# Optimization experiments

Measured on AMD Instinct MI355X. Metric: run time of the kernel, lower is better.

## Reference

```python
import jax, jax.numpy as jnp
import numpy as np
import math

B, S, D_MODEL, N_HEAD, D_HEAD, D_FFN = 1, 2048, 1024, 16, 64, 4096
EPS = 1e-6


def setup_inputs() -> dict:
    key = jax.random.key(0)
    ks = jax.random.split(key, 10)
    scale = 0.02
    x = jax.random.normal(ks[0], (B, S, D_MODEL), dtype=jnp.float32)
    # RoPE frequencies: freqs_cis[s, i] = exp(1j * s * theta_i), theta_i = 10000^{-2i/d_head}
    half = D_HEAD // 2
    inv_freq = 1.0 / (10000.0 ** (jnp.arange(0, half, dtype=jnp.float32) * 2.0 / D_HEAD))
    angles = jnp.arange(S, dtype=jnp.float32)[:, None] * inv_freq[None, :]  # [S, half]
    freqs_cos = jnp.cos(angles)
    freqs_sin = jnp.sin(angles)
    wq = jax.random.normal(ks[1], (D_MODEL, N_HEAD * D_HEAD), dtype=jnp.float32) * scale
    wk = jax.random.normal(ks[2], (D_MODEL, N_HEAD * D_HEAD), dtype=jnp.float32) * scale
    wv = jax.random.normal(ks[3], (D_MODEL, N_HEAD * D_HEAD), dtype=jnp.float32) * scale
    wo = jax.random.normal(ks[4], (N_HEAD * D_HEAD, D_MODEL), dtype=jnp.float32) * scale
    w1 = jax.random.normal(ks[5], (D_MODEL, D_FFN), dtype=jnp.float32) * scale
    w2 = jax.random.normal(ks[6], (D_FFN, D_MODEL), dtype=jnp.float32) * scale
    w3 = jax.random.normal(ks[7], (D_MODEL, D_FFN), dtype=jnp.float32) * scale
    attn_norm_w = jnp.ones((D_MODEL,), dtype=jnp.float32)
    ffn_norm_w = jnp.ones((D_MODEL,), dtype=jnp.float32)
    return {"x": x, "freqs_cos": freqs_cos, "freqs_sin": freqs_sin,
            "wq": wq, "wk": wk, "wv": wv, "wo": wo,
            "w1": w1, "w2": w2, "w3": w3,
            "attn_norm_w": attn_norm_w, "ffn_norm_w": ffn_norm_w}


def _rmsnorm(x, w):
    xf = x.astype(jnp.float32)
    inv = jax.lax.rsqrt(jnp.mean(xf * xf, axis=-1, keepdims=True) + EPS)
    return (xf * inv).astype(x.dtype) * w


def _rope(t, cos, sin):
    # t: [B, S, H, D]; treat last dim as interleaved (even, odd) complex pairs
    b, s, h, d = t.shape
    tr = t.astype(jnp.float32).reshape(b, s, h, d // 2, 2)
    te, to = tr[..., 0], tr[..., 1]
    c = cos[None, :, None, :]
    sn = sin[None, :, None, :]
    out = jnp.stack([te * c - to * sn, te * sn + to * c], axis=-1)
    return out.reshape(b, s, h, d).astype(t.dtype)


def reference(x, freqs_cos, freqs_sin, wq, wk, wv, wo, w1, w2, w3, attn_norm_w, ffn_norm_w):
    bsz, seqlen, _ = x.shape
    # --- attention sub-block ---
    hin = _rmsnorm(x, attn_norm_w)
    q = (hin @ wq).reshape(bsz, seqlen, N_HEAD, D_HEAD)
    k = (hin @ wk).reshape(bsz, seqlen, N_HEAD, D_HEAD)
    v = (hin @ wv).reshape(bsz, seqlen, N_HEAD, D_HEAD)
    q = _rope(q, freqs_cos, freqs_sin)
    k = _rope(k, freqs_cos, freqs_sin)
    # [B, H, S, S] scores, softmax in fp32 (no causal mask in original)
    scores = jnp.einsum('bqhd,bkhd->bhqk', q, k) / math.sqrt(D_HEAD)
    probs = jax.nn.softmax(scores.astype(jnp.float32), axis=-1).astype(q.dtype)
    attn = jnp.einsum('bhqk,bkhd->bqhd', probs, v).reshape(bsz, seqlen, N_HEAD * D_HEAD)
    h = x + attn @ wo
    # --- SwiGLU FFN sub-block ---
    f = _rmsnorm(h, ffn_norm_w)
    ffn = (jax.nn.silu(f @ w1) * (f @ w3)) @ w2
    return h + ffn
```

## Files before the change

kernel.cpp:

```cpp
#include <hip/hip_runtime.h>
#include <stdint.h>
#include <stddef.h>

using bf16x8 = __attribute__((ext_vector_type(8))) __bf16;
using f32x4  = __attribute__((ext_vector_type(4))) float;
using f32x16 = __attribute__((ext_vector_type(16))) float;

__device__ __forceinline__ float bf2f(unsigned short u) {
  union { unsigned int i; float f; } v; v.i = ((unsigned int)u) << 16; return v.f;
}
__device__ __forceinline__ unsigned short f2bf(float f) {
  union { float f; unsigned int i; } v; v.f = f;
  unsigned int r = v.i + 0x7fffu + ((v.i >> 16) & 1u);
  return (unsigned short)(r >> 16);
}
__device__ __forceinline__ unsigned short f2bf_trunc(float f) {
  union { float f; unsigned int i; } v; v.f = f;
  return (unsigned short)(v.i >> 16);
}
__device__ __forceinline__ void async16(const void* g, void* l) {
  __builtin_amdgcn_global_load_lds(
      (const __attribute__((address_space(1))) unsigned int*)g,
      (__attribute__((address_space(3))) unsigned int*)l, 16, 0, 0);
}

#define S_LEN 2048
#define DMODEL 1024
#define NHEAD 16
#define DHEAD 64
#define DFFN 4096

struct T4 {
  const float *s0, *s1, *s2, *s3;
  unsigned short *d0, *d1, *d2, *d3;
};
__global__ __launch_bounds__(256) void transpose4_k(T4 j) {
  const float* in = blockIdx.z == 0 ? j.s0 : blockIdx.z == 1 ? j.s1 : blockIdx.z == 2 ? j.s2 : j.s3;
  unsigned short* out = blockIdx.z == 0 ? j.d0 : blockIdx.z == 1 ? j.d1 : blockIdx.z == 2 ? j.d2 : j.d3;
  __shared__ unsigned short tile[32][33];
  const int tx = threadIdx.x & 31;
  const int ty = threadIdx.x >> 5;
  const int bc = blockIdx.x * 32;
  const int br = blockIdx.y * 32;
#pragma unroll
  for (int i = 0; i < 4; ++i)
    tile[ty + i * 8][tx] = f2bf(in[(size_t)(br + ty + i * 8) * 1024 + bc + tx]);
  __syncthreads();
#pragma unroll
  for (int i = 0; i < 4; ++i)
    out[(size_t)(bc + ty + i * 8) * 1024 + br + tx] = tile[tx][ty + i * 8];
}

__global__ __launch_bounds__(256) void transpose13_k(
    const float* __restrict__ w1, const float* __restrict__ w3,
    unsigned short* __restrict__ out) {
  const float* in = blockIdx.z ? w3 : w1;
  const int rb = blockIdx.z * 32;
  __shared__ unsigned short tile[32][33];
  const int tx = threadIdx.x & 31;
  const int ty = threadIdx.x >> 5;
  const int bc = blockIdx.x * 32;
  const int br = blockIdx.y * 32;
#pragma unroll
  for (int i = 0; i < 4; ++i)
    tile[ty + i * 8][tx] = f2bf(in[(size_t)(br + ty + i * 8) * 4096 + bc + tx]);
  __syncthreads();
#pragma unroll
  for (int i = 0; i < 4; ++i) {
    int c = bc + ty + i * 8;
    int dest = (c >> 5) * 64 + rb + (c & 31);
    out[(size_t)dest * 1024 + br + tx] = tile[tx][ty + i * 8];
  }
}

__global__ __launch_bounds__(256) void transpose_w2_k(
    const float* __restrict__ in, unsigned short* __restrict__ out) {
  __shared__ unsigned short tile[32][33];
  const int tx = threadIdx.x & 31;
  const int ty = threadIdx.x >> 5;
  const int bc = blockIdx.x * 32;
  const int br = blockIdx.y * 32;
#pragma unroll
  for (int i = 0; i < 4; ++i)
    tile[ty + i * 8][tx] = f2bf(in[(size_t)(br + ty + i * 8) * 1024 + bc + tx]);
  __syncthreads();
#pragma unroll
  for (int i = 0; i < 4; ++i)
    out[(size_t)(bc + ty + i * 8) * 4096 + br + tx] = tile[tx][ty + i * 8];
}

__global__ __launch_bounds__(256) void vtrans_k(
    const unsigned short* __restrict__ QKV, unsigned short* __restrict__ VtG) {
  __shared__ unsigned short tile[32][33];
  const int tx = threadIdx.x & 31;
  const int ty = threadIdx.x >> 5;
  const int bc = blockIdx.x * 32;
  const int br = blockIdx.y * 32;
#pragma unroll
  for (int i = 0; i < 4; ++i)
    tile[ty + i * 8][tx] = QKV[(size_t)(br + ty + i * 8) * 3072 + 2048 + bc + tx];
  __syncthreads();
#pragma unroll
  for (int i = 0; i < 4; ++i)
    VtG[(size_t)(bc + ty + i * 8) * 2048 + br + tx] = tile[tx][ty + i * 8];
}

__global__ __launch_bounds__(256) void rmsnorm_k(
    const float* __restrict__ X, const float* __restrict__ W,
    unsigned short* __restrict__ Y) {
  const int row = blockIdx.x;
  const int t = threadIdx.x;
  const int lane = t & 63, w = t >> 6;
  const float* x = X + (size_t)row * DMODEL;
  float xs[4];
  float s = 0.f;
#pragma unroll
  for (int i = 0; i < 4; ++i) {
    xs[i] = x[t * 4 + i];
    s += xs[i] * xs[i];
  }
#pragma unroll
  for (int m = 1; m < 64; m <<= 1) s += __shfl_xor(s, m, 64);
  __shared__ float red[4];
  if (lane == 0) red[w] = s;
  __syncthreads();
  float tot = red[0] + red[1] + red[2] + red[3];
  float inv = rsqrtf(tot * (1.0f / DMODEL) + 1e-6f);
#pragma unroll
  for (int i = 0; i < 4; ++i)
    Y[(size_t)row * DMODEL + t * 4 + i] = f2bf(xs[i] * inv * W[t * 4 + i]);
}

template <int MODE>
__global__ __launch_bounds__(256) void gemm_bt(
    const unsigned short* __restrict__ A, int lda,
    const unsigned short* __restrict__ BT,
    void* __restrict__ Cout,
    int K, int N) {
  __shared__ unsigned short As[128 * 64];
  __shared__ unsigned short Bs[128 * 64];
  const int t = threadIdx.x;
  const int lane = t & 63;
  const int w = t >> 6;
  const int qr = (w >> 1) * 64, qc = (w & 1) * 64;
  const int l31 = lane & 31, half = lane >> 5;
  const int m0 = blockIdx.y * 128, n0 = blockIdx.x * 128;

  f32x16 acc[2][2] = {};

  int srow[4], scol[4];
#pragma unroll
  for (int p = 0; p < 4; ++p) {
    int off = p * 2048 + t * 8;
    int r = off >> 6;
    srow[p] = r;
    scol[p] = (((off >> 3) & 7) ^ (r & 7)) * 8;
  }

  for (int k0 = 0; k0 < K; k0 += 64) {
    __syncthreads();
#pragma unroll
    for (int p = 0; p < 4; ++p) {
      int off = p * 2048 + t * 8;
      async16(A + (size_t)(m0 + srow[p]) * lda + (k0 + scol[p]), &As[off]);
      async16(BT + (size_t)(n0 + srow[p]) * K + (k0 + scol[p]), &Bs[off]);
    }
    __syncthreads();
#pragma unroll
    for (int ks = 0; ks < 4; ++ks) {
      const int ch = ((ks * 2 + half) ^ (l31 & 7)) * 8;
      bf16x8 a0 = *(const bf16x8*)&As[(qr + l31) * 64 + ch];
      bf16x8 a1 = *(const bf16x8*)&As[(qr + 32 + l31) * 64 + ch];
      bf16x8 b0 = *(const bf16x8*)&Bs[(qc + l31) * 64 + ch];
      bf16x8 b1 = *(const bf16x8*)&Bs[(qc + 32 + l31) * 64 + ch];
      acc[0][0] = __builtin_amdgcn_mfma_f32_32x32x16_bf16(a0, b0, acc[0][0], 0, 0, 0);
      acc[0][1] = __builtin_amdgcn_mfma_f32_32x32x16_bf16(a0, b1, acc[0][1], 0, 0, 0);
      acc[1][0] = __builtin_amdgcn_mfma_f32_32x32x16_bf16(a1, b0, acc[1][0], 0, 0, 0);
      acc[1][1] = __builtin_amdgcn_mfma_f32_32x32x16_bf16(a1, b1, acc[1][1], 0, 0, 0);
    }
  }

  if constexpr (MODE == 2) {
    unsigned short* C = (unsigned short*)Cout;
    const int ld = N >> 1;
#pragma unroll
    for (int rt = 0; rt < 2; ++rt)
#pragma unroll
      for (int reg = 0; reg < 16; ++reg) {
        int rr = m0 + qr + rt * 32 + (reg & 3) + 8 * (reg >> 2) + 4 * half;
        int cc = ((n0 + qc) >> 1) + l31;
        float a1v = acc[rt][0][reg];
        float a3v = acc[rt][1][reg];
        float f = a1v / (1.f + __expf(-a1v)) * a3v;
        C[(size_t)rr * ld + cc] = f2bf(f);
      }
  } else {
    unsigned short* C = (unsigned short*)Cout;
#pragma unroll
    for (int rt = 0; rt < 2; ++rt)
#pragma unroll
      for (int ct = 0; ct < 2; ++ct)
#pragma unroll
        for (int reg = 0; reg < 16; ++reg) {
          int rr = m0 + qr + rt * 32 + (reg & 3) + 8 * (reg >> 2) + 4 * half;
          int cc = n0 + qc + ct * 32 + l31;
          C[(size_t)rr * N + cc] = f2bf(acc[rt][ct][reg]);
        }
  }
}

struct PtrPair { float* p0; float* p1; };

__global__ __launch_bounds__(256) void gemm_bt_sk(
    const unsigned short* __restrict__ A, int lda,
    const unsigned short* __restrict__ BT,
    PtrPair parts, int Kc, int Ktot, int N) {
  __shared__ unsigned short As[64 * 64];
  __shared__ unsigned short Bs[128 * 64];
  const int t = threadIdx.x;
  const int lane = t & 63;
  const int w = t >> 6;
  const int qr = (w >> 1) * 32, qc = (w & 1) * 64;
  const int l31 = lane & 31, half = lane >> 5;
  const int m0 = blockIdx.y * 64, n0 = blockIdx.x * 128;
  const int kb = blockIdx.z * Kc;

  f32x16 acc[2] = {};

  for (int k0 = 0; k0 < Kc; k0 += 64) {
    __syncthreads();
#pragma unroll
    for (int p = 0; p < 2; ++p) {
      int off = p * 2048 + t * 8;
      int r = off >> 6;
      int sc = (((off >> 3) & 7) ^ (r & 7)) * 8;
      async16(A + (size_t)(m0 + r) * lda + (kb + k0 + sc), &As[off]);
    }
#pragma unroll
    for (int p = 0; p < 4; ++p) {
      int off = p * 2048 + t * 8;
      int r = off >> 6;
      int sc = (((off >> 3) & 7) ^ (r & 7)) * 8;
      async16(BT + (size_t)(n0 + r) * Ktot + (kb + k0 + sc), &Bs[off]);
    }
    __syncthreads();
#pragma unroll
    for (int ks = 0; ks < 4; ++ks) {
      const int ch = ((ks * 2 + half) ^ (l31 & 7)) * 8;
      bf16x8 a0 = *(const bf16x8*)&As[(qr + l31) * 64 + ch];
      bf16x8 b0 = *(const bf16x8*)&Bs[(qc + l31) * 64 + ch];
      bf16x8 b1 = *(const bf16x8*)&Bs[(qc + 32 + l31) * 64 + ch];
      acc[0] = __builtin_amdgcn_mfma_f32_32x32x16_bf16(a0, b0, acc[0], 0, 0, 0);
      acc[1] = __builtin_amdgcn_mfma_f32_32x32x16_bf16(a0, b1, acc[1], 0, 0, 0);
    }
  }

  float* C = blockIdx.z ? parts.p1 : parts.p0;
#pragma unroll
  for (int ct = 0; ct < 2; ++ct)
#pragma unroll
    for (int reg = 0; reg < 16; ++reg) {
      int rr = m0 + qr + (reg & 3) + 8 * (reg >> 2) + 4 * half;
      int cc = n0 + qc + ct * 32 + l31;
      C[(size_t)rr * N + cc] = acc[ct][reg];
    }
}

__global__ __launch_bounds__(256) void reduce2_k(
    const float4* __restrict__ P0, const float4* __restrict__ P1,
    const float4* __restrict__ R, float4* __restrict__ Out, int nvec) {
  int i = blockIdx.x * 256 + threadIdx.x;
  if (i >= nvec) return;
  float4 a = P0[i], b = P1[i], r = R[i];
  float4 o;
  o.x = a.x + b.x + r.x;
  o.y = a.y + b.y + r.y;
  o.z = a.z + b.z + r.z;
  o.w = a.w + b.w + r.w;
  Out[i] = o;
}

__global__ __launch_bounds__(256) void rope_k(
    unsigned short* __restrict__ QKV,
    const float* __restrict__ cosp,
    const float* __restrict__ sinp) {
  int idx = blockIdx.x * 256 + threadIdx.x;
  int s = idx >> 9;
  int rem = idx & 511;
  int h = rem >> 5;
  int i = rem & 31;
  float c = cosp[s * 32 + i];
  float sn = sinp[s * 32 + i];
  size_t off = (size_t)s * 3072 + h * 64 + 2 * i;
  {
    float e = bf2f(QKV[off]), o = bf2f(QKV[off + 1]);
    QKV[off] = f2bf(e * c - o * sn);
    QKV[off + 1] = f2bf(e * sn + o * c);
  }
  {
    float e = bf2f(QKV[off + 1024]), o = bf2f(QKV[off + 1025]);
    QKV[off + 1024] = f2bf((e * c - o * sn) * 0.125f);
    QKV[off + 1025] = f2bf((e * sn + o * c) * 0.125f);
  }
}

#define VPAD 132
__device__ __forceinline__ int swz(int row, int col) { return col ^ ((row & 7) * 8); }

__global__ __launch_bounds__(256) void attn_k(
    const unsigned short* __restrict__ QKV,
    const unsigned short* __restrict__ VtG,
    float* __restrict__ O0, float* __restrict__ O1,
    float* __restrict__ L) {
  const int h = blockIdx.y;
  const int qb = blockIdx.x;
  const int z = blockIdx.z;
  const int t = threadIdx.x;
  const int lane = t & 63;
  const int w = t >> 6;
  const int row16 = lane & 15, quad = lane >> 4;
  const int q0 = qb * 64 + w * 16;
  const int kbase = z * 1024;

  __shared__ unsigned short Ks[128 * 64];
  __shared__ unsigned short Vt[64 * 128];
  __shared__ unsigned short Ps[4][16 * VPAD];

  const unsigned short* Qp = QKV;
  const unsigned short* Kp = QKV + 1024;
  const unsigned short* Vg = VtG + (size_t)h * 64 * 2048;

  bf16x8 aq[2];
#pragma unroll
  for (int kk = 0; kk < 2; ++kk)
    aq[kk] = *(const bf16x8*)(Qp + (size_t)(q0 + row16) * 3072 + h * 64 + kk * 32 + quad * 8);

  f32x4 o[4] = {};
  float l_r[4] = {0.f, 0.f, 0.f, 0.f};

  bf16x8 kreg[4], vreg[4];
#pragma unroll
  for (int p = 0; p < 4; ++p) {
    int off = p * 2048 + t * 8;
    int r = off >> 6, c = off & 63;
    kreg[p] = *(const bf16x8*)(Kp + (size_t)(kbase + r) * 3072 + h * 64 + c);
    int d = off >> 7, key = off & 127;
    vreg[p] = *(const bf16x8*)(Vg + (size_t)d * 2048 + kbase + key);
  }

  for (int kb = kbase; kb < kbase + 1024; kb += 128) {
    __syncthreads();
#pragma unroll
    for (int p = 0; p < 4; ++p) {
      int off = p * 2048 + t * 8;
      int r = off >> 6, c = off & 63;
      *(bf16x8*)&Ks[r * 64 + swz(r, c)] = kreg[p];
      int d = off >> 7, key = off & 127;
      *(bf16x8*)&Vt[d * 128 + swz(d, key)] = vreg[p];
    }
    __syncthreads();
    if (kb + 128 < kbase + 1024) {
      int kb2 = kb + 128;
#pragma unroll
      for (int p = 0; p < 4; ++p) {
        int off = p * 2048 + t * 8;
        int r = off >> 6, c = off & 63;
        kreg[p] = *(const bf16x8*)(Kp + (size_t)(kb2 + r) * 3072 + h * 64 + c);
        int d = off >> 7, key = off & 127;
        vreg[p] = *(const bf16x8*)(Vg + (size_t)d * 2048 + kb2 + key);
      }
    }

    f32x4 sc[8];
#pragma unroll
    for (int tj = 0; tj < 8; ++tj) {
      int kr = tj * 16 + row16;
      bf16x8 b0 = *(const bf16x8*)&Ks[kr * 64 + swz(kr, quad * 8)];
      bf16x8 b1 = *(const bf16x8*)&Ks[kr * 64 + swz(kr, 32 + quad * 8)];
      f32x4 z4 = {};
      z4 = __builtin_amdgcn_mfma_f32_16x16x32_bf16(aq[0], b0, z4, 0, 0, 0);
      z4 = __builtin_amdgcn_mfma_f32_16x16x32_bf16(aq[1], b1, z4, 0, 0, 0);
      sc[tj] = z4;
    }

#pragma unroll
    for (int reg = 0; reg < 4; ++reg) {
      float ssum = 0.f;
#pragma unroll
      for (int tj = 0; tj < 8; ++tj) {
        float p = __expf(sc[tj][reg]);
        sc[tj][reg] = p;
        ssum += p;
      }
#pragma unroll
      for (int m = 1; m < 16; m <<= 1) ssum += __shfl_xor(ssum, m, 16);
      l_r[reg] += ssum;
    }

#pragma unroll
    for (int tj = 0; tj < 8; ++tj)
#pragma unroll
      for (int reg = 0; reg < 4; ++reg)
        Ps[w][(quad * 4 + reg) * VPAD + tj * 16 + row16] = f2bf_trunc(sc[tj][reg]);

    bf16x8 ap[4];
#pragma unroll
    for (int kk = 0; kk < 4; ++kk)
      ap[kk] = *(const bf16x8*)&Ps[w][row16 * VPAD + kk * 32 + quad * 8];
#pragma unroll
    for (int dt = 0; dt < 4; ++dt) {
      int dr = dt * 16 + row16;
#pragma unroll
      for (int kk = 0; kk < 4; ++kk) {
        bf16x8 bv = *(const bf16x8*)&Vt[dr * 128 + swz(dr, kk * 32 + quad * 8)];
        o[dt] = __builtin_amdgcn_mfma_f32_16x16x32_bf16(ap[kk], bv, o[dt], 0, 0, 0);
      }
    }
  }

  float* Op = z ? O1 : O0;
#pragma unroll
  for (int dt = 0; dt < 4; ++dt)
#pragma unroll
    for (int reg = 0; reg < 4; ++reg)
      Op[(size_t)(q0 + quad * 4 + reg) * DMODEL + h * 64 + dt * 16 + row16] = o[dt][reg];
  if (row16 == 0)
#pragma unroll
    for (int reg = 0; reg < 4; ++reg)
      L[(size_t)(h * 2 + z) * S_LEN + q0 + quad * 4 + reg] = l_r[reg];
}

__global__ __launch_bounds__(256) void attn_combine_k(
    const float4* __restrict__ O0, const float4* __restrict__ O1,
    const float* __restrict__ L, unsigned short* __restrict__ Attn) {
  int i = blockIdx.x * 256 + threadIdx.x;
  int e0 = i * 4;
  int s = e0 >> 10;
  int c = e0 & 1023;
  int h = c >> 6;
  float la = L[(size_t)(h * 2) * S_LEN + s];
  float lb = L[(size_t)(h * 2 + 1) * S_LEN + s];
  float inv = 1.f / (la + lb);
  float4 a = O0[i], b = O1[i];
  ushort4 r;
  r.x = f2bf((a.x + b.x) * inv);
  r.y = f2bf((a.y + b.y) * inv);
  r.z = f2bf((a.z + b.z) * inv);
  r.w = f2bf((a.w + b.w) * inv);
  *(ushort4*)(Attn + e0) = r;
}

extern "C" void kernel_launch(void* const* d_in, const int* in_sizes, int n_in,
                              void* d_out, int out_size, void* d_ws, size_t ws_size,
                              hipStream_t stream) {
  (void)in_sizes; (void)n_in; (void)out_size; (void)ws_size;
  const float* x    = (const float*)d_in[0];
  const float* fcos = (const float*)d_in[1];
  const float* fsin = (const float*)d_in[2];
  const float* wq   = (const float*)d_in[3];
  const float* wk   = (const float*)d_in[4];
  const float* wv   = (const float*)d_in[5];
  const float* wo   = (const float*)d_in[6];
  const float* w1   = (const float*)d_in[7];
  const float* w2   = (const float*)d_in[8];
  const float* w3   = (const float*)d_in[9];
  const float* anw  = (const float*)d_in[10];
  const float* fnw  = (const float*)d_in[11];
  float* out = (float*)d_out;
  char* ws = (char*)d_ws;

  unsigned short* WqkvT = (unsigned short*)(ws + 0);
  unsigned short* VtG   = (unsigned short*)(ws + 0);
  float*          Lbuf  = (float*)(ws + 4194304);
  unsigned short* WoT   = (unsigned short*)(ws + 6291456);
  unsigned short* QKV   = (unsigned short*)(ws + 8388608);
  unsigned short* Attn  = (unsigned short*)(ws + 20971520);
  float* Oa             = (float*)(ws + 25165824);
  float* Ob             = (float*)(ws + 37748736);
  float* P0a            = (float*)(ws + 8388608);
  float* P1a            = (float*)(ws + 25165824);
  unsigned short* F     = (unsigned short*)(ws + 0);
  float* P0b            = (float*)(ws + 16777216);
  float* P1b            = (float*)(ws + 25165824);
  unsigned short* Hin   = (unsigned short*)(ws + 33554432);
  float*          Hres  = (float*)        (ws + 37748736);
  unsigned short* W13I  = (unsigned short*)(ws + 46137344);
  unsigned short* W2T   = (unsigned short*)(ws + 62914560);

  transpose4_k<<<dim3(32, 32, 4), 256, 0, stream>>>(
      T4{wq, wk, wv, wo, WqkvT, WqkvT + 1048576, WqkvT + 2097152, WoT});
  transpose13_k<<<dim3(128, 32, 2), 256, 0, stream>>>(w1, w3, W13I);
  transpose_w2_k<<<dim3(32, 128), 256, 0, stream>>>(w2, W2T);

  rmsnorm_k<<<2048, 256, 0, stream>>>(x, anw, Hin);
  gemm_bt<0><<<dim3(24, 16), 256, 0, stream>>>(Hin, 1024, WqkvT, QKV, 1024, 3072);
  rope_k<<<4096, 256, 0, stream>>>(QKV, fcos, fsin);
  vtrans_k<<<dim3(32, 64), 256, 0, stream>>>(QKV, VtG);
  attn_k<<<dim3(32, 16, 2), 256, 0, stream>>>(QKV, VtG, Oa, Ob, Lbuf);
  attn_combine_k<<<2048, 256, 0, stream>>>((const float4*)Oa, (const float4*)Ob, Lbuf, Attn);
  gemm_bt_sk<<<dim3(8, 32, 2), 256, 0, stream>>>(Attn, 1024, WoT, PtrPair{P0a, P1a}, 512, 1024, 1024);
  reduce2_k<<<2048, 256, 0, stream>>>((const float4*)P0a, (const float4*)P1a,
                                      (const float4*)x, (float4*)Hres, 524288);

  rmsnorm_k<<<2048, 256, 0, stream>>>(Hres, fnw, Hin);
  gemm_bt<2><<<dim3(64, 16), 256, 0, stream>>>(Hin, 1024, W13I, F, 1024, 8192);
  gemm_bt_sk<<<dim3(8, 32, 2), 256, 0, stream>>>(F, 4096, W2T, PtrPair{P0b, P1b}, 2048, 4096, 1024);
  reduce2_k<<<2048, 256, 0, stream>>>((const float4*)P0b, (const float4*)P1b,
                                      (const float4*)Hres, (float4*)out, 524288);
}
```

Measured before the change: 314.7 us.

## Replace W1/W3 SwiGLU GEMM with 256x256-tile double-buffered pipelined kernel

Swaps the 128x128-tile FFN up-projection GEMM (with fused SiLU-gate epilogue) for a new 512-thread kernel that uses 256x256 output tiles, a double-buffered 128KB LDS ring fed by async global-to-LDS loads, and interleaves the staging of the next K-tile with MFMA phases separated by barriers and s_setprio. It also remaps block indices so neighbouring blocks share A and B panels. The intent is more data reuse per loaded byte and overlap of memory traffic with matrix math. In exchange, occupancy drops to one large block per CU with heavy LDS use, there are only 256 blocks, and the hand-written wait counts and barrier schedule are fragile.

New measurement: 309.4 us. No clear change (-1.7%).

```diff
diff --git a/kernel.cpp b/kernel.cpp
--- a/kernel.cpp
+++ b/kernel.cpp
@@ -180,21 +180,7 @@
     }
   }
 
-  if constexpr (MODE == 2) {
-    unsigned short* C = (unsigned short*)Cout;
-    const int ld = N >> 1;
-#pragma unroll
-    for (int rt = 0; rt < 2; ++rt)
-#pragma unroll
-      for (int reg = 0; reg < 16; ++reg) {
-        int rr = m0 + qr + rt * 32 + (reg & 3) + 8 * (reg >> 2) + 4 * half;
-        int cc = ((n0 + qc) >> 1) + l31;
-        float a1v = acc[rt][0][reg];
-        float a3v = acc[rt][1][reg];
-        float f = a1v / (1.f + __expf(-a1v)) * a3v;
-        C[(size_t)rr * ld + cc] = f2bf(f);
-      }
-  } else {
+  {
     unsigned short* C = (unsigned short*)Cout;
 #pragma unroll
     for (int rt = 0; rt < 2; ++rt)
@@ -207,6 +193,162 @@
           C[(size_t)rr * N + cc] = f2bf(acc[rt][ct][reg]);
         }
   }
+}
+
+__device__ __forceinline__ void mfma8(f32x16& c0, f32x16& c1,
+                                      const bf16x8 (&a)[2][4],
+                                      const bf16x8 (&b)[4]) {
+  __builtin_amdgcn_s_setprio(1);
+#pragma unroll
+  for (int ks = 0; ks < 4; ++ks) {
+    c0 = __builtin_amdgcn_mfma_f32_32x32x16_bf16(a[0][ks], b[ks], c0, 0, 0, 0);
+    c1 = __builtin_amdgcn_mfma_f32_32x32x16_bf16(a[1][ks], b[ks], c1, 0, 0, 0);
+  }
+  __builtin_amdgcn_s_setprio(0);
+}
+
+__global__ __launch_bounds__(512, 2) void gemm256_silu(
+    const unsigned short* __restrict__ A,
+    const unsigned short* __restrict__ BT,
+    unsigned short* __restrict__ F) {
+  __shared__ unsigned short lds[65536];
+  const int t = threadIdx.x;
+  const int l = t & 63, l31 = l & 31, half = l >> 5;
+  const int w = t >> 6;
+  const int wm = w >> 2, wn = w & 3;
+
+  const int orig = blockIdx.x;
+  const int bx = (orig & 7) * 4 + ((orig >> 3) & 3);
+  const int by = orig >> 5;
+  const int m0 = by * 256, n0 = bx * 256;
+
+  const int rA = t >> 3;
+  const int sc = ((t & 7) ^ ((t >> 3) & 7)) * 8;
+  const int lo = t * 8;
+
+#define STAGE_A(h, tile, d)                                                    \
+  { async16(A + (size_t)(m0 + (h) * 128 + rA) * 1024 + (tile) * 64 + sc,       \
+            &lds[(d) * 32768 + (h) * 8192 + lo]);                              \
+    async16(A + (size_t)(m0 + (h) * 128 + 64 + rA) * 1024 + (tile) * 64 + sc,  \
+            &lds[(d) * 32768 + (h) * 8192 + 4096 + lo]); }
+#define STAGE_B(h, tile, d)                                                    \
+  { async16(BT + (size_t)(n0 + (h) * 128 + rA) * 1024 + (tile) * 64 + sc,      \
+            &lds[(d) * 32768 + 16384 + (h) * 8192 + lo]);                      \
+    async16(BT + (size_t)(n0 + (h) * 128 + 64 + rA) * 1024 + (tile) * 64 + sc, \
+            &lds[(d) * 32768 + 16384 + (h) * 8192 + 4096 + lo]); }
+
+  const int arow = wm * 128 + l31;
+  const int brow = wn * 64 + l31;
+  int kc[4];
+#pragma unroll
+  for (int ks = 0; ks < 4; ++ks) kc[ks] = ((ks * 2 + half) ^ (l31 & 7)) * 8;
+
+#define LDA(d, mt, ks) (*(const bf16x8*)&lds[(d) * 32768 + (arow + (mt) * 32) * 64 + kc[ks]])
+#define LDB(d, nt, ks) (*(const bf16x8*)&lds[(d) * 32768 + 16384 + (brow + (nt) * 32) * 64 + kc[ks]])
+
+  f32x16 acc[4][2] = {};
+  bf16x8 afr[2][4], bfr[2][4];
+
+  STAGE_A(0, 0, 0); STAGE_A(1, 0, 0); STAGE_B(0, 0, 0); STAGE_B(1, 0, 0);
+  STAGE_A(0, 1, 1);
+  asm volatile("s_waitcnt vmcnt(2)" ::: "memory");
+  __builtin_amdgcn_s_barrier();
+
+#pragma unroll 1
+  for (int i = 0; i < 8; ++i) {
+    const int t1 = 2 * i + 1, t2 = 2 * i + 2, t3 = 2 * i + 3;
+    const bool more = i < 7;
+
+#pragma unroll
+    for (int ks = 0; ks < 4; ++ks) {
+      afr[0][ks] = LDA(0, 0, ks);
+      afr[1][ks] = LDA(0, 1, ks);
+      bfr[0][ks] = LDB(0, 0, ks);
+    }
+    STAGE_A(1, t1, 1);
+    __builtin_amdgcn_s_barrier();
+    mfma8(acc[0][0], acc[1][0], afr, bfr[0]);
+    __builtin_amdgcn_s_barrier();
+
+#pragma unroll
+    for (int ks = 0; ks < 4; ++ks) bfr[1][ks] = LDB(0, 1, ks);
+    STAGE_B(0, t1, 1);
+    __builtin_amdgcn_s_barrier();
+    mfma8(acc[0][1], acc[1][1], afr, bfr[1]);
+    __builtin_amdgcn_s_barrier();
+
+#pragma unroll
+    for (int ks = 0; ks < 4; ++ks) {
+      afr[0][ks] = LDA(0, 2, ks);
+      afr[1][ks] = LDA(0, 3, ks);
+    }
+    STAGE_B(1, t1, 1);
+    __builtin_amdgcn_s_barrier();
+    mfma8(acc[2][1], acc[3][1], afr, bfr[1]);
+    __builtin_amdgcn_s_barrier();
+
+    if (more) {
+      STAGE_A(0, t2, 0);
+      asm volatile("s_waitcnt vmcnt(2)" ::: "memory");
+    } else {
+      asm volatile("s_waitcnt vmcnt(0)" ::: "memory");
+    }
+    __builtin_amdgcn_s_barrier();
+    mfma8(acc[2][0], acc[3][0], afr, bfr[0]);
+    __builtin_amdgcn_s_barrier();
+
+#pragma unroll
+    for (int ks = 0; ks < 4; ++ks) {
+      afr[0][ks] = LDA(1, 0, ks);
+      afr[1][ks] = LDA(1, 1, ks);
+      bfr[0][ks] = LDB(1, 0, ks);
+    }
+    if (more) STAGE_A(1, t2, 0);
+    __builtin_amdgcn_s_barrier();
+    mfma8(acc[0][0], acc[1][0], afr, bfr[0]);
+    __builtin_amdgcn_s_barrier();
+
+#pragma unroll
+    for (int ks = 0; ks < 4; ++ks) bfr[1][ks] = LDB(1, 1, ks);
+    if (more) STAGE_B(0, t2, 0);
+    __builtin_amdgcn_s_barrier();
+    mfma8(acc[0][1], acc[1][1], afr, bfr[1]);
+    __builtin_amdgcn_s_barrier();
+
+#pragma unroll
+    for (int ks = 0; ks < 4; ++ks) {
+      afr[0][ks] = LDA(1, 2, ks);
+      afr[1][ks] = LDA(1, 3, ks);
+    }
+    if (more) STAGE_B(1, t2, 0);
+    __builtin_amdgcn_s_barrier();
+    mfma8(acc[2][1], acc[3][1], afr, bfr[1]);
+    __builtin_amdgcn_s_barrier();
+
+    if (more) STAGE_A(0, t3, 1);
+    asm volatile("s_waitcnt vmcnt(2)" ::: "memory");
+    __builtin_amdgcn_s_barrier();
+    mfma8(acc[2][0], acc[3][0], afr, bfr[0]);
+    __builtin_amdgcn_s_barrier();
+  }
+
+#undef STAGE_A
+#undef STAGE_B
+#undef LDA
+#undef LDB
+
+  const int ccol = (n0 >> 1) + wn * 32 + l31;
+  const int rbase = m0 + wm * 128 + 4 * half;
+#pragma unroll
+  for (int mt = 0; mt < 4; ++mt)
+#pragma unroll
+    for (int reg = 0; reg < 16; ++reg) {
+      int rr = rbase + mt * 32 + (reg & 3) + 8 * (reg >> 2);
+      float a1v = acc[mt][0][reg];
+      float a3v = acc[mt][1][reg];
+      float f = a1v / (1.f + __expf(-a1v)) * a3v;
+      F[(size_t)rr * 4096 + ccol] = f2bf(f);
+    }
 }
 
 struct PtrPair { float* p0; float* p1; };
@@ -503,7 +645,7 @@
                                       (const float4*)x, (float4*)Hres, 524288);
 
   rmsnorm_k<<<2048, 256, 0, stream>>>(Hres, fnw, Hin);
-  gemm_bt<2><<<dim3(64, 16), 256, 0, stream>>>(Hin, 1024, W13I, F, 1024, 8192);
+  gemm256_silu<<<dim3(256), 512, 0, stream>>>(Hin, W13I, F);
   gemm_bt_sk<<<dim3(8, 32, 2), 256, 0, stream>>>(F, 4096, W2T, PtrPair{P0b, P1b}, 2048, 4096, 1024);
   reduce2_k<<<2048, 256, 0, stream>>>((const float4*)P0b, (const float4*)P1b,
                                       (const float4*)Hres, (float4*)out, 524288);
```
